# Kernel tuning notes

Measured on AMD Instinct MI355X. Metric: run time of the kernel, lower is better.

## Reference

```python
import jax, jax.numpy as jnp
import numpy as np

EPS = 1e-7        # Hyperboloid.eps for float32
MIN_NORM = 1e-15
MAX_NORM = 1e6
K = 1.0           # c = 1 -> K = 1/c
SQRT_K = 1.0
SLOPE = 0.01      # nn.LeakyReLU default negative_slope


def _cosh(x):
    return jnp.cosh(jnp.clip(x, -15.0, 15.0))


def _sinh(x):
    return jnp.sinh(jnp.clip(x, -15.0, 15.0))


def _arcosh(x):
    x = jnp.clip(x, 1.0 + 1e-7)
    return jnp.log(x + jnp.sqrt(x * x - 1.0))


def _norm(y):
    # safe row-norm (grad-finite at 0); original clamps norm to >=1e-15 anyway
    return jnp.sqrt(jnp.clip(jnp.sum(y * y, axis=-1, keepdims=True), 1e-30))


def mdot(x, y):
    return jnp.sum(x * y, axis=-1, keepdims=True) - 2.0 * x[..., :1] * y[..., :1]


def mnorm(u):
    return jnp.sqrt(jnp.clip(mdot(u, u), EPS))


def proj(x):
    y = x[..., 1:]
    x0 = jnp.sqrt(jnp.clip(K + jnp.sum(y * y, axis=-1, keepdims=True), EPS))
    return jnp.concatenate([x0, y], axis=-1)


def proj_tan0(u):
    return jnp.concatenate([jnp.zeros_like(u[..., :1]), u[..., 1:]], axis=-1)


def proj_tan(u, x):
    ux = jnp.sum(x[..., 1:] * u[..., 1:], axis=-1, keepdims=True)
    v0 = ux / jnp.clip(x[..., :1], EPS)
    return jnp.concatenate([v0, u[..., 1:]], axis=-1)


def expmap0(u):
    y = u[..., 1:]
    yn = jnp.clip(_norm(y), MIN_NORM)
    theta = yn / SQRT_K
    r0 = SQRT_K * _cosh(theta)
    r = SQRT_K * _sinh(theta) * y / yn
    return proj(jnp.concatenate([r0, r], axis=-1))


def logmap0(x):
    y = x[..., 1:]
    yn = jnp.clip(_norm(y), MIN_NORM)
    theta = jnp.clip(x[..., :1] / SQRT_K, 1.0 + EPS)
    r = SQRT_K * _arcosh(theta) * y / yn
    return jnp.concatenate([jnp.zeros_like(x[..., :1]), r], axis=-1)


def expmap(u, x):
    nu = jnp.clip(mnorm(u), None, MAX_NORM)
    theta = jnp.clip(nu / SQRT_K, MIN_NORM)
    return proj(_cosh(theta) * x + _sinh(theta) * u / theta)


def ptransp0(x, u):
    x0 = x[..., :1]
    y = x[..., 1:]
    yn = jnp.clip(_norm(y), MIN_NORM)
    y_hat = y / yn
    v = jnp.concatenate([-yn, (SQRT_K - x0) * y_hat], axis=-1)
    alpha = jnp.sum(y_hat * u[..., 1:], axis=-1, keepdims=True) / SQRT_K
    return proj_tan(u - alpha * v, x)


def mobius_add(x, y):
    u = logmap0(y)
    v = ptransp0(x, u)
    return expmap(v, x)


def hgcn_forward(x, adj, weight, bias):
    # map Euclidean input to the hyperboloid (HGCN.encode prologue)
    xh = proj(expmap0(proj_tan0(x)))
    # HypLinear: mobius_matvec (logmap0 -> matmul -> expmap0) + hyperbolic bias add
    res = proj(expmap0(logmap0(xh) @ weight.T))
    hyp_bias = proj(expmap0(proj_tan0(bias[None, :])))
    res = proj(mobius_add(res, hyp_bias))
    # HypAgg (use_att=False): aggregate in tangent space at origin via spmm
    h = proj(expmap0(adj @ logmap0(res)))
    # HypAct: LeakyReLU in tangent space, then back to hyperboloid
    t = proj_tan0(jax.nn.leaky_relu(logmap0(h), SLOPE))
    return proj(expmap0(t))


def setup_inputs() -> dict:
    key = jax.random.key(0)
    k1, k2, k3, k4 = jax.random.split(key, 4)
    N, D = 8192, 64
    x = jax.random.normal(k1, (N, D), dtype=jnp.float32)
    adj = jax.random.uniform(k2, (N, N), dtype=jnp.float32)
    adj = adj / jnp.sum(adj, axis=1, keepdims=True)  # row-normalized dense adjacency
    weight = jax.random.uniform(k3, (D, D), dtype=jnp.float32)  # init.uniform_ in [0,1)
    bias = 0.01 * jax.random.normal(k4, (D,), dtype=jnp.float32)
    return {"x": x, "adj": adj, "weight": weight, "bias": bias}


def reference(x, adj, weight, bias):
    return hgcn_forward(x, adj, weight, bias)
```

## Files before the change

kernel.cpp:

```cpp
#include <hip/hip_runtime.h>
#include <hip/hip_bf16.h>
#include <math.h>

typedef __bf16 bf16x8 __attribute__((ext_vector_type(8)));
typedef __bf16 bf16x4 __attribute__((ext_vector_type(4)));
typedef float  f32x4  __attribute__((ext_vector_type(4)));

#define NND 8192
#define DIM 64
#define PB  10368

__device__ __forceinline__ float wsum(float v) {
#pragma unroll
    for (int m = 1; m < 64; m <<= 1) v += __shfl_xor(v, m, 64);
    return v;
}

struct SC { float sh, ch; };
__device__ __forceinline__ SC sinhcosh(float c) {
    float e  = expf(c);
    float ei = 1.0f / e;
    SC r; r.sh = 0.5f * (e - ei); r.ch = 0.5f * (e + ei);
    return r;
}

__device__ __forceinline__ float arcosh_from_n2(float n2) {
    float t = fmaxf(n2, 2.0000001e-7f);
    return logf(sqrtf(1.0f + t) + sqrtf(t));
}

__device__ __forceinline__ float tangent_chain(float xv, int lane) {
    float y   = (lane == 0) ? 0.0f : xv;
    float yn2 = wsum(y * y);
    float yn  = fmaxf(sqrtf(fmaxf(yn2, 1e-30f)), 1e-15f);
    SC s1 = sinhcosh(fminf(yn, 15.0f));
    float r   = (lane == 0) ? 0.0f : s1.sh * y / yn;
    float rn2 = wsum(r * r);
    float ynb = fmaxf(sqrtf(fmaxf(rn2, 1e-30f)), 1e-15f);
    float ac  = arcosh_from_n2(rn2);
    return (lane == 0) ? 0.0f : ac * r / ynb;
}

__device__ __forceinline__ float second_chain(float m, float ubv, float theta_b, int lane) {
    float my  = (lane == 0) ? 0.0f : m;
    float mn2 = wsum(my * my);
    float mn  = fmaxf(sqrtf(fmaxf(mn2, 1e-30f)), 1e-15f);
    SC s2 = sinhcosh(fminf(mn, 15.0f));
    float rr   = (lane == 0) ? 0.0f : s2.sh * my / mn;
    float rrn2 = wsum(rr * rr);
    float res0 = sqrtf(fmaxf(1.0f + rrn2, 1e-7f));
    float yn3   = fmaxf(sqrtf(fmaxf(rrn2, 1e-30f)), 1e-15f);
    float yhat  = (lane == 0) ? 0.0f : rr / yn3;
    float alpha = wsum(yhat * ubv);
    float w_    = ubv - alpha * (1.0f - res0) * yhat;
    float ux    = wsum(rr * w_);
    float v0    = ux / fmaxf(res0, 1e-7f);
    float vv    = (lane == 0) ? v0 : w_;
    float resv  = (lane == 0) ? res0 : rr;
    float theta = theta_b;
    SC s3 = sinhcosh(fminf(theta, 15.0f));
    float pv  = s3.ch * resv + s3.sh * vv / theta;
    float pn2 = wsum((lane == 0) ? 0.0f : pv * pv);
    float yn4 = fmaxf(sqrtf(fmaxf(pn2, 1e-30f)), 1e-15f);
    float ac4 = arcosh_from_n2(pn2);
    return (lane == 0) ? 0.0f : ac4 * pv / yn4;
}

__device__ __forceinline__ float epilogue_chain(float hv, int lane) {
    float y   = (lane == 0) ? 0.0f : hv;
    float yn2 = wsum(y * y);
    float yn  = fmaxf(sqrtf(fmaxf(yn2, 1e-30f)), 1e-15f);
    SC s1 = sinhcosh(fminf(yn, 15.0f));
    float r   = (lane == 0) ? 0.0f : s1.sh * y / yn;
    float rn2 = wsum(r * r);
    float ynb = fmaxf(sqrtf(fmaxf(rn2, 1e-30f)), 1e-15f);
    float ac  = arcosh_from_n2(rn2);
    float lgv = (lane == 0) ? 0.0f : ac * r / ynb;
    float t   = (lgv > 0.0f) ? lgv : 0.01f * lgv;
    float tn2 = wsum(t * t);
    float tn  = fmaxf(sqrtf(fmaxf(tn2, 1e-30f)), 1e-15f);
    SC s3 = sinhcosh(fminf(tn, 15.0f));
    float ov  = (lane == 0) ? 0.0f : s3.sh * t / tn;
    float on2 = wsum(ov * ov);
    float o0  = sqrtf(fmaxf(1.0f + on2, 1e-7f));
    return (lane == 0) ? o0 : ov;
}

__global__ __launch_bounds__(256) void k_prep(
    const float* __restrict__ x, const float* __restrict__ weight,
    const float* __restrict__ bias, __bf16* __restrict__ l2bf)
{
    __shared__ float WL[64][65];
    const int tid  = threadIdx.x;
    const int lane = tid & 63;
    const int wave = tid >> 6;
#pragma unroll
    for (int i = 0; i < 16; ++i) {
        int idx = i * 256 + tid;
        WL[idx >> 6][idx & 63] = weight[idx];
    }
    __syncthreads();
    float ubv  = tangent_chain(bias[lane], lane);
    float nub2 = wsum(ubv * ubv);
    float thb  = fmaxf(fminf(sqrtf(fmaxf(nub2, 1e-7f)), 1e6f), 1e-15f);

    const int row = blockIdx.x * 4 + wave;
    float xv  = x[row * 64 + lane];
    float L1v = tangent_chain(xv, lane);
    float mj0 = 0.f, mj1 = 0.f, mj2 = 0.f, mj3 = 0.f;
#pragma unroll
    for (int d = 0; d < 64; d += 4) {
        mj0 = fmaf(__shfl(L1v, d,     64), WL[lane][d],     mj0);
        mj1 = fmaf(__shfl(L1v, d + 1, 64), WL[lane][d + 1], mj1);
        mj2 = fmaf(__shfl(L1v, d + 2, 64), WL[lane][d + 2], mj2);
        mj3 = fmaf(__shfl(L1v, d + 3, 64), WL[lane][d + 3], mj3);
    }
    float mj  = (mj0 + mj1) + (mj2 + mj3);
    float L2v = second_chain(mj, ubv, thb, lane);
    l2bf[(size_t)lane * PB + row] = (__bf16)L2v;
}

#define ISSUE_A(T, V)  V = *reinterpret_cast<const f32x4*>(gA + (T) * 64);
#define WRITE_A(T, V)  do {                                                     \
    bf16x4 p_; p_[0]=(__bf16)V[0]; p_[1]=(__bf16)V[1];                          \
    p_[2]=(__bf16)V[2]; p_[3]=(__bf16)V[3];                                     \
    *reinterpret_cast<bf16x4*>(As[(T) & 1] + aw_idx) = p_;                      \
} while (0)
#define COMPUTE(T) do {                                                         \
    _Pragma("unroll")                                                           \
    for (int s_ = 0; s_ < 2; ++s_) {                                            \
        bf16x8 a_ = *reinterpret_cast<const bf16x8*>(                           \
            As[(T) & 1] + ar_row * 64 + (((4 * s_ + lg) ^ lx7) * 8));           \
        bf16x8 b_ = *reinterpret_cast<const bf16x8*>(                           \
            Bs + br_row * 256 + (((((T) & 3) * 8 + 4 * s_ + lg) ^ lx7) * 8));   \
        acc = __builtin_amdgcn_mfma_f32_16x16x32_bf16(a_, b_, acc, 0, 0, 0);    \
    }                                                                           \
} while (0)
#define STAGE_B(HALF) do {                                                      \
    _Pragma("unroll")                                                           \
    for (int i_ = 0; i_ < 4; ++i_) {                                            \
        const int f_ = i_ * 512 + tid;                                          \
        const int r_ = f_ >> 5, c_ = f_ & 31;                                   \
        vb[i_] = *reinterpret_cast<const bf16x8*>(                              \
            l2bf + (size_t)r_ * PB + kc + (HALF) * 256 + c_ * 8);               \
    }                                                                           \
} while (0)
#define WRITE_B() do {                                                          \
    _Pragma("unroll")                                                           \
    for (int i_ = 0; i_ < 4; ++i_) {                                            \
        const int f_ = i_ * 512 + tid;                                          \
        const int r_ = f_ >> 5, c_ = f_ & 31;                                   \
        *reinterpret_cast<bf16x8*>(Bs + r_ * 256 + ((c_ ^ (r_ & 7)) * 8)) = vb[i_]; \
    }                                                                           \
} while (0)

__global__ __launch_bounds__(512, 6) void k_mm(
    const float* __restrict__ adj, const __bf16* __restrict__ l2bf,
    float* __restrict__ pws)
{
    __shared__ __bf16 Bs[64 * 256];
    __shared__ __bf16 As[2][32 * 64];
    const int tid  = threadIdx.x;
    const int lane = tid & 63;
    const int w    = tid >> 6;
    const int l15  = lane & 15;
    const int lg   = lane >> 4;
    const int lx7  = l15 & 7;
    const int rh   = w >> 2;
    const int dq   = w & 3;
    const int rg   = blockIdx.x & 255;
    const int kch  = blockIdx.x >> 8;
    const int R0   = rg * 32;
    const int kc   = kch * 512;

    const int arow = tid >> 4;
    const int acol = (tid & 15) * 4;
    const int aw_idx = arow * 64 + (((acol >> 3) ^ (arow & 7)) * 8) + (acol & 7);
    const int ar_row = rh * 16 + l15;
    const int br_row = dq * 16 + l15;
    const float* gA = adj + (size_t)(R0 + arow) * NND + kc + acol;

    f32x4 va0, va1;
    bf16x8 vb[4];
    f32x4 acc = {0.f, 0.f, 0.f, 0.f};

    STAGE_B(0);
    ISSUE_A(0, va0);
    WRITE_B();
    WRITE_A(0, va0);
    ISSUE_A(1, va1);
    __syncthreads();

    ISSUE_A(2, va0); COMPUTE(0); WRITE_A(1, va1); __syncthreads();
    ISSUE_A(3, va1); COMPUTE(1); WRITE_A(2, va0); __syncthreads();
    ISSUE_A(4, va0); STAGE_B(1); COMPUTE(2); WRITE_A(3, va1); __syncthreads();
    ISSUE_A(5, va1); COMPUTE(3); __syncthreads();
    WRITE_A(4, va0); WRITE_B(); __syncthreads();
    ISSUE_A(6, va0); COMPUTE(4); WRITE_A(5, va1); __syncthreads();
    ISSUE_A(7, va1); COMPUTE(5); WRITE_A(6, va0); __syncthreads();
    COMPUTE(6); WRITE_A(7, va1); __syncthreads();
    COMPUTE(7);

    float* pp = pws + (size_t)kch * NND * DIM;
#pragma unroll
    for (int i = 0; i < 4; ++i) {
        pp[(size_t)(R0 + rh * 16 + lg * 4 + i) * DIM + dq * 16 + l15] = acc[i];
    }
}

__global__ __launch_bounds__(256) void k_fin(
    const float* __restrict__ pws, float* __restrict__ out)
{
    const int tid  = threadIdx.x;
    const int lane = tid & 63;
    const int wave = tid >> 6;
    const int row  = blockIdx.x * 4 + wave;
    const size_t base = (size_t)row * DIM + lane;
    const size_t S = (size_t)NND * DIM;
    float hv = 0.0f;
#pragma unroll
    for (int s = 0; s < 16; ++s) hv += pws[s * S + base];
    out[base] = epilogue_chain(hv, lane);
}

extern "C" void kernel_launch(void* const* d_in, const int* in_sizes, int n_in,
                              void* d_out, int out_size, void* d_ws, size_t ws_size,
                              hipStream_t stream)
{
    const float* x      = (const float*)d_in[0];
    const float* adj    = (const float*)d_in[1];
    const float* weight = (const float*)d_in[2];
    const float* bias   = (const float*)d_in[3];
    float* out = (float*)d_out;
    __bf16* l2bf = (__bf16*)d_ws;
    float*  pws  = (float*)((char*)d_ws + 0x180000);

    k_prep<<<2048, 256, 0, stream>>>(x, weight, bias, l2bf);
    k_mm<<<4096, 512, 0, stream>>>(adj, l2bf, pws);
    k_fin<<<2048, 256, 0, stream>>>(pws, out);
}
```

Before: 92.19 us.

## Double split-K chunk length, halve partial sums, deepen A prefetch to three buffers

```diff
diff --git a/kernel.cpp b/kernel.cpp
--- a/kernel.cpp
+++ b/kernel.cpp
@@ -136,13 +136,13 @@
         acc = __builtin_amdgcn_mfma_f32_16x16x32_bf16(a_, b_, acc, 0, 0, 0);    \
     }                                                                           \
 } while (0)
-#define STAGE_B(HALF) do {                                                      \
+#define STAGE_B(Q) do {                                                         \
     _Pragma("unroll")                                                           \
     for (int i_ = 0; i_ < 4; ++i_) {                                            \
         const int f_ = i_ * 512 + tid;                                          \
         const int r_ = f_ >> 5, c_ = f_ & 31;                                   \
         vb[i_] = *reinterpret_cast<const bf16x8*>(                              \
-            l2bf + (size_t)r_ * PB + kc + (HALF) * 256 + c_ * 8);               \
+            l2bf + (size_t)r_ * PB + kc + (Q) * 256 + c_ * 8);                  \
     }                                                                           \
 } while (0)
 #define WRITE_B() do {                                                          \
@@ -171,7 +171,7 @@
     const int rg   = blockIdx.x & 255;
     const int kch  = blockIdx.x >> 8;
     const int R0   = rg * 32;
-    const int kc   = kch * 512;
+    const int kc   = kch * 1024;
 
     const int arow = tid >> 4;
     const int acol = (tid & 15) * 4;
@@ -180,26 +180,36 @@
     const int br_row = dq * 16 + l15;
     const float* gA = adj + (size_t)(R0 + arow) * NND + kc + acol;
 
-    f32x4 va0, va1;
+    f32x4 va0, va1, va2;
     bf16x8 vb[4];
     f32x4 acc = {0.f, 0.f, 0.f, 0.f};
 
     STAGE_B(0);
-    ISSUE_A(0, va0);
+    ISSUE_A(0, va0); ISSUE_A(1, va1); ISSUE_A(2, va2);
     WRITE_B();
     WRITE_A(0, va0);
-    ISSUE_A(1, va1);
+    ISSUE_A(3, va0);
     __syncthreads();
 
-    ISSUE_A(2, va0); COMPUTE(0); WRITE_A(1, va1); __syncthreads();
-    ISSUE_A(3, va1); COMPUTE(1); WRITE_A(2, va0); __syncthreads();
-    ISSUE_A(4, va0); STAGE_B(1); COMPUTE(2); WRITE_A(3, va1); __syncthreads();
-    ISSUE_A(5, va1); COMPUTE(3); __syncthreads();
-    WRITE_A(4, va0); WRITE_B(); __syncthreads();
-    ISSUE_A(6, va0); COMPUTE(4); WRITE_A(5, va1); __syncthreads();
-    ISSUE_A(7, va1); COMPUTE(5); WRITE_A(6, va0); __syncthreads();
-    COMPUTE(6); WRITE_A(7, va1); __syncthreads();
-    COMPUTE(7);
+    COMPUTE(0);                WRITE_A(1, va1);  ISSUE_A(4, va1);  __syncthreads();
+    COMPUTE(1);  STAGE_B(1);   WRITE_A(2, va2);  ISSUE_A(5, va2);  __syncthreads();
+    COMPUTE(2);                WRITE_A(3, va0);  ISSUE_A(6, va0);  __syncthreads();
+    COMPUTE(3);  __syncthreads();  WRITE_B();
+                               WRITE_A(4, va1);  ISSUE_A(7, va1);  __syncthreads();
+    COMPUTE(4);                WRITE_A(5, va2);  ISSUE_A(8, va2);  __syncthreads();
+    COMPUTE(5);  STAGE_B(2);   WRITE_A(6, va0);  ISSUE_A(9, va0);  __syncthreads();
+    COMPUTE(6);                WRITE_A(7, va1);  ISSUE_A(10, va1); __syncthreads();
+    COMPUTE(7);  __syncthreads();  WRITE_B();
+                               WRITE_A(8, va2);  ISSUE_A(11, va2); __syncthreads();
+    COMPUTE(8);                WRITE_A(9, va0);  ISSUE_A(12, va0); __syncthreads();
+    COMPUTE(9);  STAGE_B(3);   WRITE_A(10, va1); ISSUE_A(13, va1); __syncthreads();
+    COMPUTE(10);               WRITE_A(11, va2); ISSUE_A(14, va2); __syncthreads();
+    COMPUTE(11); __syncthreads();  WRITE_B();
+                               WRITE_A(12, va0); ISSUE_A(15, va0); __syncthreads();
+    COMPUTE(12);               WRITE_A(13, va1);                   __syncthreads();
+    COMPUTE(13);               WRITE_A(14, va2);                   __syncthreads();
+    COMPUTE(14);               WRITE_A(15, va0);                   __syncthreads();
+    COMPUTE(15);
 
     float* pp = pws + (size_t)kch * NND * DIM;
 #pragma unroll
@@ -217,9 +227,8 @@
     const int row  = blockIdx.x * 4 + wave;
     const size_t base = (size_t)row * DIM + lane;
     const size_t S = (size_t)NND * DIM;
-    float hv = 0.0f;
-#pragma unroll
-    for (int s = 0; s < 16; ++s) hv += pws[s * S + base];
+    float hv = (((pws[base] + pws[S + base]) + (pws[2*S + base] + pws[3*S + base]))
+             +  ((pws[4*S + base] + pws[5*S + base]) + (pws[6*S + base] + pws[7*S + base])));
     out[base] = epilogue_chain(hv, lane);
 }
 
@@ -236,6 +245,6 @@
     float*  pws  = (float*)((char*)d_ws + 0x180000);
 
     k_prep<<<2048, 256, 0, stream>>>(x, weight, bias, l2bf);
-    k_mm<<<4096, 512, 0, stream>>>(adj, l2bf, pws);
+    k_mm<<<2048, 512, 0, stream>>>(adj, l2bf, pws);
     k_fin<<<2048, 256, 0, stream>>>(pws, out);
 }
```

New measurement: 79.61 us. -13.6%, faster.
